# Kernel tuning notes

Hardware: AMD Instinct MI355X
Metric: run time of the kernel (lower is better)

Reference implementation:

```python
import jax, jax.numpy as jnp
import numpy as np
from jax import lax

B, N, S = 16, 8192, 512
BASE_K = 16
MS_K = (8, 16, 24)


def _fps(xyz, npoint):
    # farthest point sampling; xyz [B,N,3] -> indices [B,npoint]
    b, n, _ = xyz.shape
    def body(carry, _):
        dists, far = carry
        c = jnp.take_along_axis(xyz, far[:, None, None], axis=1)  # [B,1,3]
        d = jnp.sum((xyz - c) ** 2, -1)
        dists = jnp.minimum(dists, d)
        return (dists, jnp.argmax(dists, -1).astype(jnp.int32)), far
    init = (jnp.full((b, n), 1e10, xyz.dtype), jnp.zeros((b,), jnp.int32))
    _, idx = lax.scan(body, init, None, length=npoint)
    return idx.swapaxes(0, 1)  # [B,npoint]


def _sqdist(a, b):
    # a [B,S,3], b [B,N,3] -> squared distances [B,S,N] (same topk order as cdist)
    return (jnp.sum(a * a, -1)[:, :, None] + jnp.sum(b * b, -1)[:, None, :]
            - 2.0 * jnp.einsum('bsc,bnc->bsn', a, b))


def _gather(pts, idx):
    # pts [B,N,C], idx [B,S,K] -> [B,S,K,C]
    b = pts.shape[0]
    return pts[jnp.arange(b)[:, None, None], idx]


def setup_inputs():
    key = jax.random.key(0)
    ks = jax.random.split(key, 6)
    s = 0.05
    return {
        'l0_xyz': jax.random.normal(ks[0], (B, 3, N), jnp.float32),
        'l0_points': jax.random.normal(ks[1], (B, 3, N), jnp.float32),
        'sa_W1': jax.random.normal(ks[2], (64, 6), jnp.float32) * s,
        'sa_b1': jnp.zeros((64,), jnp.float32),
        'sa_W2': jax.random.normal(ks[3], (128, 64), jnp.float32) * s,
        'sa_b2': jnp.zeros((128,), jnp.float32),
        'ms_W1': jax.random.normal(ks[4], (3, 64, 3), jnp.float32) * s,
        'ms_b1': jnp.zeros((3, 64), jnp.float32),
        'ms_W2': jax.random.normal(ks[5], (3, 128, 64), jnp.float32) * s,
        'ms_b2': jnp.zeros((3, 128), jnp.float32),
    }


def reference(l0_xyz, l0_points, sa_W1, sa_b1, sa_W2, sa_b2, ms_W1, ms_b1, ms_W2, ms_b2):
    xyz = l0_xyz.swapaxes(1, 2)     # [B,N,3]
    pts = l0_points.swapaxes(1, 2)  # [B,N,3]
    # --- PointNet_SA_Module_KNN: FPS + KNN grouping + shared MLP + max-pool ---
    fps_idx = _fps(lax.stop_gradient(xyz), S)                         # [B,S]
    new_xyz = jnp.take_along_axis(xyz, fps_idx[:, :, None], axis=1)  # [B,S,3]
    d = _sqdist(lax.stop_gradient(new_xyz), lax.stop_gradient(xyz))  # [B,S,N]
    _, knn_idx = lax.top_k(-d, BASE_K)                                # [B,S,K]
    g_xyz = _gather(xyz, knn_idx) - new_xyz[:, :, None]               # [B,S,K,3]
    g_pts = _gather(pts, knn_idx)                                     # [B,S,K,3]
    feat = jnp.concatenate([g_xyz, g_pts], -1)                        # [B,S,K,6]
    h = jax.nn.relu(jnp.einsum('bskc,oc->bsko', feat, sa_W1) + sa_b1)
    h = jnp.einsum('bsko,po->bskp', h, sa_W2) + sa_b2
    base_feat = jnp.max(h, axis=2)                                    # [B,S,128]
    keypoints = new_xyz.swapaxes(1, 2)                                # [B,3,S]
    # --- multi-scale: no_grad cdist, per-scale topk + rel-coord MLP + max-pool ---
    dist = _sqdist(lax.stop_gradient(new_xyz), lax.stop_gradient(xyz))  # [B,S,N]
    feats = [base_feat.swapaxes(1, 2)]                                  # [B,128,S]
    for i, k in enumerate(MS_K):
        k_eff = min(k, N)
        _, idx = lax.top_k(-dist, k_eff)                                # [B,S,k]
        rel = _gather(xyz, idx) - new_xyz[:, :, None]                   # [B,S,k,3]
        h = jax.nn.relu(jnp.einsum('bskc,oc->bsko', rel, ms_W1[i]) + ms_b1[i])
        h = jnp.einsum('bsko,po->bskp', h, ms_W2[i]) + ms_b2[i]
        feats.append(jnp.max(h, axis=2).swapaxes(1, 2))                 # [B,128,S]
    return keypoints, jnp.concatenate(feats, axis=1)                    # [B,3,S],[B,512,S]
```

## Files before the change

### kernel.cpp

```cpp
#include <hip/hip_runtime.h>

#define BB 16
#define NN 8192
#define SS 512
#define N3 (3 * NN)
#define KD 14

typedef unsigned short u16;
typedef unsigned int u32;
typedef unsigned long long u64;
typedef float v2f __attribute__((ext_vector_type(2)));

__device__ __forceinline__ v2f pk_add(v2f a, v2f b) {
  v2f r;
  asm("v_pk_add_f32 %0, %1, %2" : "=v"(r) : "v"(a), "v"(b));
  return r;
}
__device__ __forceinline__ v2f pk_mul(v2f a, v2f b) {
  v2f r;
  asm("v_pk_mul_f32 %0, %1, %2" : "=v"(r) : "v"(a), "v"(b));
  return r;
}

template <int CTRL>
__device__ __forceinline__ u64 dpp_maxk(u64 k) {
  u32 lo = (u32)k, hi = (u32)(k >> 32);
  u32 slo = (u32)__builtin_amdgcn_update_dpp(0, (int)lo, CTRL, 0xf, 0xf, false);
  u32 shi = (u32)__builtin_amdgcn_update_dpp(0, (int)hi, CTRL, 0xf, 0xf, false);
  u64 s = ((u64)shi << 32) | (u64)slo;
  return (s > k) ? s : k;
}
__device__ __forceinline__ u64 maxk(u64 a, u64 b) { return (a > b) ? a : b; }

__global__ __launch_bounds__(256) void k_prep(const float* __restrict__ xyz,
                                              const float* __restrict__ pts,
                                              float4* __restrict__ xyz4,
                                              float4* __restrict__ pts4) {
  int i = blockIdx.x * 256 + threadIdx.x;
  int b = i >> 13, n = i & (NN - 1);
  const float* xb = xyz + b * N3;
  float x = xb[n], y = xb[NN + n], z = xb[2 * NN + n];
  float w = __fadd_rn(__fadd_rn(__fmul_rn(x, x), __fmul_rn(y, y)), __fmul_rn(z, z));
  xyz4[i] = make_float4(x, y, z, w);
  const float* pb = pts + b * N3;
  pts4[i] = make_float4(pb[n], pb[NN + n], pb[2 * NN + n], 0.f);
}

__global__ __attribute__((amdgpu_flat_work_group_size(512, 512),
                          amdgpu_waves_per_eu(2, 2)))
void k_fps(const float* __restrict__ xyz, float* __restrict__ out_kp) {
  __shared__ float sxyz[NN * 3];
  __shared__ int sIdx[SS];
  __shared__ u64 rkey[2][8];
  int b = blockIdx.x, t = threadIdx.x;
  const float* base = xyz + b * N3;
  v2f px[8], py[8], pz[8], dm[8];
#pragma unroll
  for (int j = 0; j < 8; ++j) {
    int n0 = j * 1024 + t, n1 = n0 + 512;
    px[j] = v2f{base[n0], base[n1]};
    py[j] = v2f{base[NN + n0], base[NN + n1]};
    pz[j] = v2f{base[2 * NN + n0], base[2 * NN + n1]};
    dm[j] = v2f{1e10f, 1e10f};
    sxyz[n0 * 3 + 0] = px[j].x;
    sxyz[n0 * 3 + 1] = py[j].x;
    sxyz[n0 * 3 + 2] = pz[j].x;
    sxyz[n1 * 3 + 0] = px[j].y;
    sxyz[n1 * 3 + 1] = py[j].y;
    sxyz[n1 * 3 + 2] = pz[j].y;
  }
#pragma unroll
  for (int j = 0; j < 8; ++j) {
    asm volatile("" : "+v"(px[j]), "+v"(py[j]), "+v"(pz[j]));
  }
  float cx = base[0], cy = base[NN], cz = base[2 * NN];
  int far = 0;
  int lane = t & 63, w = t >> 6;
  u32 tb = (u32)(NN - t);
  for (int it = 0; it < SS; ++it) {
    if (t == 0) sIdx[it] = far;
    v2f ncx = v2f{-cx, -cx}, ncy = v2f{-cy, -cy}, ncz = v2f{-cz, -cz};
    float vmax = 0.0f;
#pragma unroll
    for (int j = 0; j < 8; ++j) {
      v2f dx = pk_add(px[j], ncx);
      v2f dy = pk_add(py[j], ncy);
      v2f dz = pk_add(pz[j], ncz);
      v2f xx = pk_mul(dx, dx);
      v2f yy = pk_mul(dy, dy);
      v2f s = pk_add(xx, yy);
      v2f zz = pk_mul(dz, dz);
      v2f d = pk_add(s, zz);
      float a0 = fminf(dm[j].x, d.x);
      float a1 = fminf(dm[j].y, d.y);
      dm[j].x = a0;
      dm[j].y = a1;
      vmax = fmaxf(vmax, fmaxf(a0, a1));
    }
    u32 cand = 0;
#pragma unroll
    for (int j = 7; j >= 0; --j) {
      u32 v1 = tb - (u32)(j * 1024 + 512);
      u32 v0 = tb - (u32)(j * 1024);
      cand = (dm[j].y == vmax) ? v1 : cand;
      cand = (dm[j].x == vmax) ? v0 : cand;
    }
    u64 key = ((u64)__float_as_uint(vmax) << 32) | cand;
    key = dpp_maxk<0x111>(key);
    key = dpp_maxk<0x112>(key);
    key = dpp_maxk<0x114>(key);
    key = dpp_maxk<0x118>(key);
    key = dpp_maxk<0x142>(key);
    key = dpp_maxk<0x143>(key);
    int pb = it & 1;
    if (lane == 63) rkey[pb][w] = key;
    __syncthreads();
    u64 k0 = rkey[pb][0], k1 = rkey[pb][1];
    u64 k2 = rkey[pb][2], k3 = rkey[pb][3];
    u64 k4 = rkey[pb][4], k5 = rkey[pb][5];
    u64 k6 = rkey[pb][6], k7 = rkey[pb][7];
    u64 kg = maxk(maxk(maxk(k0, k1), maxk(k2, k3)),
                  maxk(maxk(k4, k5), maxk(k6, k7)));
    far = NN - (int)(u32)(kg & 0xffffffffu);
    cx = sxyz[far * 3 + 0];
    cy = sxyz[far * 3 + 1];
    cz = sxyz[far * 3 + 2];
  }
  __syncthreads();
  for (int i = t; i < SS; i += 512) {
    int id = sIdx[i];
    out_kp[b * 1536 + i] = base[id];
    out_kp[b * 1536 + SS + i] = base[NN + id];
    out_kp[b * 1536 + 2 * SS + i] = base[2 * NN + id];
  }
}

template <int USE4>
__global__ __launch_bounds__(256) void k_knn(const float* __restrict__ xyz,
                                             const float4* __restrict__ xyz4,
                                             const float* __restrict__ kp,
                                             u16* __restrict__ knn) {
  int t = threadIdx.x;
  int row = blockIdx.x * 4 + (t >> 6);
  int lane = t & 63;
  int b = row >> 9, s = row & (SS - 1);
  const float* base = xyz + b * N3;
  const float4* base4 = xyz4 + (b << 13);
  float ax = kp[b * 1536 + s];
  float ay = kp[b * 1536 + SS + s];
  float az = kp[b * 1536 + 2 * SS + s];
  float aw = __fadd_rn(__fadd_rn(__fmul_rn(ax, ax), __fmul_rn(ay, ay)), __fmul_rn(az, az));
  u64 arr[KD];
#pragma unroll
  for (int i = 0; i < KD; ++i) arr[i] = ~0ull;
  for (int c = 0; c < 128; ++c) {
    int n = c * 64 + lane;
    float qx, qy, qz, qw;
    if constexpr (USE4) {
      float4 q = base4[n];
      qx = q.x; qy = q.y; qz = q.z; qw = q.w;
    } else {
      qx = base[n]; qy = base[NN + n]; qz = base[2 * NN + n];
      qw = __fadd_rn(__fadd_rn(__fmul_rn(qx, qx), __fmul_rn(qy, qy)), __fmul_rn(qz, qz));
    }
    float dot = __fadd_rn(__fadd_rn(__fmul_rn(ax, qx), __fmul_rn(ay, qy)), __fmul_rn(az, qz));
    float d = __fsub_rn(__fadd_rn(aw, qw), __fmul_rn(2.0f, dot));
    u32 ub = __float_as_uint(d);
    ub ^= (ub & 0x80000000u) ? 0xFFFFFFFFu : 0x80000000u;
    u64 key = ((u64)ub << 32) | (u32)n;
    if (key < arr[KD - 1]) {
      bool cg[KD];
#pragma unroll
      for (int i = 0; i < KD; ++i) cg[i] = arr[i] > key;
#pragma unroll
      for (int i = KD - 1; i >= 1; --i)
        arr[i] = cg[i - 1] ? arr[i - 1] : (cg[i] ? key : arr[i]);
      arr[0] = cg[0] ? key : arr[0];
    }
  }
  u64 mine = 0;
  for (int it = 0; it < 24; ++it) {
    u64 m = arr[0];
#pragma unroll
    for (int off = 1; off < 64; off <<= 1) {
      u64 o = __shfl_xor(m, off, 64);
      m = (o < m) ? o : m;
    }
    if (lane == it) mine = m;
    if (arr[0] == m) {
#pragma unroll
      for (int i = 0; i < KD - 1; ++i) arr[i] = arr[i + 1];
      arr[KD - 1] = ~0ull;
    }
  }
  if (lane < 24) knn[row * 24 + lane] = (u16)(mine & 0xFFFFu);
}

template <int USE4>
__global__ __launch_bounds__(256) void k_mlp(
    const float* __restrict__ xyz, const float* __restrict__ pts,
    const float4* __restrict__ xyz4, const float4* __restrict__ pts4,
    const float* __restrict__ kp, const u16* __restrict__ knn,
    const float* __restrict__ W1, const float* __restrict__ b1,
    const float* __restrict__ W2, const float* __restrict__ b2,
    const float* __restrict__ msW1, const float* __restrict__ msb1,
    const float* __restrict__ msW2, const float* __restrict__ msb2,
    float* __restrict__ out) {
  __shared__ float smem[6688];
  int t = threadIdx.x, lane = t & 63, w = t >> 6;
  int b = blockIdx.x >> 6, s0 = (blockIdx.x & 63) * 8;
  if (blockIdx.y == 0) {
    float* sW1T = smem;
    float* sb1 = smem + 384;
    float* sfeat = smem + 448;
    float* sh1 = smem + 832;
    for (int i = t; i < 384; i += 256) {
      int o = i / 6, c = i - o * 6;
      sW1T[c * 64 + o] = W1[i];
    }
    if (t < 64) sb1[t] = b1[t];
    float wgtA[64], wgtB[64];
#pragma unroll
    for (int j = 0; j < 64; ++j) {
      wgtA[j] = W2[lane * 64 + j];
      wgtB[j] = W2[(lane + 64) * 64 + j];
    }
    float b2A = b2[lane], b2B = b2[lane + 64];
    __syncthreads();
    for (int g = 0; g < 2; ++g) {
      if (t < 128) {
        int p = t >> 1, h = t & 1;
        int rr = p >> 4, k = p & 15;
        int s = s0 + g * 4 + rr, row = b * SS + s;
        int id = knn[row * 24 + k];
        float* f = &sfeat[rr * 96 + k * 6];
        if (h == 0) {
          float qx, qy, qz;
          if constexpr (USE4) {
            float4 q = xyz4[(b << 13) + id];
            qx = q.x; qy = q.y; qz = q.z;
          } else {
            qx = xyz[b * N3 + id];
            qy = xyz[b * N3 + NN + id];
            qz = xyz[b * N3 + 2 * NN + id];
          }
          f[0] = __fsub_rn(qx, kp[b * 1536 + s]);
          f[1] = __fsub_rn(qy, kp[b * 1536 + SS + s]);
          f[2] = __fsub_rn(qz, kp[b * 1536 + 2 * SS + s]);
        } else {
          float px_, py_, pz_;
          if constexpr (USE4) {
            float4 q = pts4[(b << 13) + id];
            px_ = q.x; py_ = q.y; pz_ = q.z;
          } else {
            px_ = pts[b * N3 + id];
            py_ = pts[b * N3 + NN + id];
            pz_ = pts[b * N3 + 2 * NN + id];
          }
          f[3] = px_;
          f[4] = py_;
          f[5] = pz_;
        }
      }
      __syncthreads();
#pragma unroll
      for (int m = 0; m < 16; ++m) {
        int u = m * 256 + t;
        int rr = u >> 10, rem = u & 1023, k = rem >> 6, o = rem & 63;
        float acc = sb1[o];
#pragma unroll
        for (int c = 0; c < 6; ++c) acc = fmaf(sfeat[rr * 96 + k * 6 + c], sW1T[c * 64 + o], acc);
        sh1[rr * 1024 + k * 64 + o] = fmaxf(acc, 0.f);
      }
      __syncthreads();
      float bestA = -1e30f, bestB = -1e30f;
#pragma unroll
      for (int k = 0; k < 16; ++k) {
        const float4* h4 = (const float4*)&sh1[w * 1024 + k * 64];
        float a0 = 0.f, a1 = 0.f;
#pragma unroll
        for (int j = 0; j < 16; ++j) {
          float4 hv = h4[j];
          a0 = fmaf(hv.x, wgtA[4 * j], a0);
          a0 = fmaf(hv.y, wgtA[4 * j + 1], a0);
          a0 = fmaf(hv.z, wgtA[4 * j + 2], a0);
          a0 = fmaf(hv.w, wgtA[4 * j + 3], a0);
          a1 = fmaf(hv.x, wgtB[4 * j], a1);
          a1 = fmaf(hv.y, wgtB[4 * j + 1], a1);
          a1 = fmaf(hv.z, wgtB[4 * j + 2], a1);
          a1 = fmaf(hv.w, wgtB[4 * j + 3], a1);
        }
        bestA = fmaxf(bestA, a0);
        bestB = fmaxf(bestB, a1);
      }
      int s = s0 + g * 4 + w;
      out[24576 + b * 262144 + lane * 512 + s] = bestA + b2A;
      out[24576 + b * 262144 + (lane + 64) * 512 + s] = bestB + b2B;
      __syncthreads();
    }
  } else {
    int scale = blockIdx.y - 1;
    int kk = 8 * (scale + 1);
    float* sW1T = smem;
    float* sb1 = smem + 192;
    float* sfeat = smem + 256;
    float* sh1 = smem + 544;
    const float* W1s = msW1 + scale * 192;
    for (int i = t; i < 192; i += 256) {
      int o = i / 3, c = i - o * 3;
      sW1T[c * 64 + o] = W1s[i];
    }
    if (t < 64) sb1[t] = msb1[scale * 64 + t];
    float wgtA[64], wgtB[64];
#pragma unroll
    for (int j = 0; j < 64; ++j) {
      wgtA[j] = msW2[scale * 8192 + lane * 64 + j];
      wgtB[j] = msW2[scale * 8192 + (lane + 64) * 64 + j];
    }
    float b2A = msb2[scale * 128 + lane], b2B = msb2[scale * 128 + lane + 64];
    __syncthreads();
    int co = 128 * (scale + 1);
    for (int g = 0; g < 2; ++g) {
      if (t < 96) {
        int rr = t / 24, k = t - rr * 24;
        int s = s0 + g * 4 + rr, row = b * SS + s;
        int id = knn[row * 24 + k];
        float qx, qy, qz;
        if constexpr (USE4) {
          float4 q = xyz4[(b << 13) + id];
          qx = q.x; qy = q.y; qz = q.z;
        } else {
          qx = xyz[b * N3 + id];
          qy = xyz[b * N3 + NN + id];
          qz = xyz[b * N3 + 2 * NN + id];
        }
        float* f = &sfeat[rr * 72 + k * 3];
        f[0] = __fsub_rn(qx, kp[b * 1536 + s]);
        f[1] = __fsub_rn(qy, kp[b * 1536 + SS + s]);
        f[2] = __fsub_rn(qz, kp[b * 1536 + 2 * SS + s]);
      }
      __syncthreads();
      for (int rr = 0; rr < 4; ++rr) {
        for (int u = t; u < kk * 64; u += 256) {
          int k = u >> 6, o = u & 63;
          float acc = sb1[o];
          acc = fmaf(sfeat[rr * 72 + k * 3 + 0], sW1T[o], acc);
          acc = fmaf(sfeat[rr * 72 + k * 3 + 1], sW1T[64 + o], acc);
          acc = fmaf(sfeat[rr * 72 + k * 3 + 2], sW1T[128 + o], acc);
          sh1[rr * 1536 + k * 64 + o] = fmaxf(acc, 0.f);
        }
      }
      __syncthreads();
      float bestA = -1e30f, bestB = -1e30f;
      for (int k = 0; k < kk; ++k) {
        const float4* h4 = (const float4*)&sh1[w * 1536 + k * 64];
        float a0 = 0.f, a1 = 0.f;
#pragma unroll
        for (int j = 0; j < 16; ++j) {
          float4 hv = h4[j];
          a0 = fmaf(hv.x, wgtA[4 * j], a0);
          a0 = fmaf(hv.y, wgtA[4 * j + 1], a0);
          a0 = fmaf(hv.z, wgtA[4 * j + 2], a0);
          a0 = fmaf(hv.w, wgtA[4 * j + 3], a0);
          a1 = fmaf(hv.x, wgtB[4 * j], a1);
          a1 = fmaf(hv.y, wgtB[4 * j + 1], a1);
          a1 = fmaf(hv.z, wgtB[4 * j + 2], a1);
          a1 = fmaf(hv.w, wgtB[4 * j + 3], a1);
        }
        bestA = fmaxf(bestA, a0);
        bestB = fmaxf(bestB, a1);
      }
      int s = s0 + g * 4 + w;
      out[24576 + b * 262144 + (co + lane) * 512 + s] = bestA + b2A;
      out[24576 + b * 262144 + (co + lane + 64) * 512 + s] = bestB + b2B;
      __syncthreads();
    }
  }
}

extern "C" void kernel_launch(void* const* d_in, const int* in_sizes, int n_in,
                              void* d_out, int out_size, void* d_ws, size_t ws_size,
                              hipStream_t stream) {
  const float* xyz = (const float*)d_in[0];
  const float* pts = (const float*)d_in[1];
  const float* sa_W1 = (const float*)d_in[2];
  const float* sa_b1 = (const float*)d_in[3];
  const float* sa_W2 = (const float*)d_in[4];
  const float* sa_b2 = (const float*)d_in[5];
  const float* ms_W1 = (const float*)d_in[6];
  const float* ms_b1 = (const float*)d_in[7];
  const float* ms_W2 = (const float*)d_in[8];
  const float* ms_b2 = (const float*)d_in[9];
  float* out = (float*)d_out;
  const float* kp = (const float*)d_out;

  u16* knn = (u16*)d_ws;
  float4* xyz4 = (float4*)((char*)d_ws + 393216);
  float4* pts4 = xyz4 + BB * NN;
  const size_t need4 = 393216 + (size_t)2 * BB * NN * sizeof(float4);
  const bool use4 = ws_size >= need4;

  if (use4) k_prep<<<BB * NN / 256, 256, 0, stream>>>(xyz, pts, xyz4, pts4);
  k_fps<<<BB, 512, 0, stream>>>(xyz, out);
  if (use4) {
    k_knn<1><<<(BB * SS) / 4, 256, 0, stream>>>(xyz, xyz4, kp, knn);
    k_mlp<1><<<dim3(BB * 64, 4), 256, 0, stream>>>(xyz, pts, xyz4, pts4, kp, knn,
                                                   sa_W1, sa_b1, sa_W2, sa_b2,
                                                   ms_W1, ms_b1, ms_W2, ms_b2, out);
  } else {
    k_knn<0><<<(BB * SS) / 4, 256, 0, stream>>>(xyz, xyz4, kp, knn);
    k_mlp<0><<<dim3(BB * 64, 4), 256, 0, stream>>>(xyz, pts, xyz4, pts4, kp, knn,
                                                   sa_W1, sa_b1, sa_W2, sa_b2,
                                                   ms_W1, ms_b1, ms_W2, ms_b2, out);
  }
}
```

Measured before the change: 967.1 us.

## Fuse FPS and KNN into one persistent kernel with progress flags

FPS and KNN now run in a single launch. The 16 FPS blocks publish each sampled keypoint and bump a per-batch progress counter. The extra 128 worker blocks spin on those counters and compute top-k neighbours for each keypoint as soon as it exists. This overlaps the serial FPS loop with the KNN work, instead of running KNN only after all of FPS finishes. It relies on all blocks being co-resident (there is a deadlock risk if they are not), and it adds global stores, memory fences and spin-wait traffic inside the FPS loop.

```diff
diff --git a/kernel.cpp b/kernel.cpp
--- a/kernel.cpp
+++ b/kernel.cpp
@@ -5,6 +5,8 @@
 #define SS 512
 #define N3 (3 * NN)
 #define KD 14
+#define KNN_BLOCKS 128
+#define KNN_WAVES (KNN_BLOCKS * 8)
 
 typedef unsigned short u16;
 typedef unsigned int u32;
@@ -35,7 +37,11 @@
 __global__ __launch_bounds__(256) void k_prep(const float* __restrict__ xyz,
                                               const float* __restrict__ pts,
                                               float4* __restrict__ xyz4,
-                                              float4* __restrict__ pts4) {
+                                              float4* __restrict__ pts4,
+                                              u32* __restrict__ progress) {
+  if (blockIdx.x == 0 && threadIdx.x < BB)
+    __hip_atomic_store(progress + threadIdx.x, 0u, __ATOMIC_RELAXED,
+                       __HIP_MEMORY_SCOPE_AGENT);
   int i = blockIdx.x * 256 + threadIdx.x;
   int b = i >> 13, n = i & (NN - 1);
   const float* xb = xyz + b * N3;
@@ -48,7 +54,169 @@
 
 __global__ __attribute__((amdgpu_flat_work_group_size(512, 512),
                           amdgpu_waves_per_eu(2, 2)))
-void k_fps(const float* __restrict__ xyz, float* __restrict__ out_kp) {
+void k_fps_knn(const float* __restrict__ xyz, const float4* __restrict__ xyz4,
+               float* __restrict__ out_kp, u16* __restrict__ knn,
+               u32* __restrict__ progress) {
+  __shared__ float sxyz[NN * 3];
+  __shared__ u64 rkey[2][8];
+  int t = threadIdx.x;
+  int lane = t & 63, w = t >> 6;
+  if (blockIdx.x < BB) {
+    int b = blockIdx.x;
+    const float* base = xyz + b * N3;
+    v2f px[8], py[8], pz[8], dm[8];
+#pragma unroll
+    for (int j = 0; j < 8; ++j) {
+      int n0 = j * 1024 + t, n1 = n0 + 512;
+      px[j] = v2f{base[n0], base[n1]};
+      py[j] = v2f{base[NN + n0], base[NN + n1]};
+      pz[j] = v2f{base[2 * NN + n0], base[2 * NN + n1]};
+      dm[j] = v2f{1e10f, 1e10f};
+      sxyz[n0 * 3 + 0] = px[j].x;
+      sxyz[n0 * 3 + 1] = py[j].x;
+      sxyz[n0 * 3 + 2] = pz[j].x;
+      sxyz[n1 * 3 + 0] = px[j].y;
+      sxyz[n1 * 3 + 1] = py[j].y;
+      sxyz[n1 * 3 + 2] = pz[j].y;
+    }
+#pragma unroll
+    for (int j = 0; j < 8; ++j) {
+      asm volatile("" : "+v"(px[j]), "+v"(py[j]), "+v"(pz[j]));
+    }
+    float cx = base[0], cy = base[NN], cz = base[2 * NN];
+    u32 tb = (u32)(NN - t);
+    for (int it = 0; it < SS; ++it) {
+      if (t == 0) {
+        if (it > 0) {
+          asm volatile("s_waitcnt vmcnt(0)" ::: "memory");
+          __hip_atomic_store(progress + b, (u32)it, __ATOMIC_RELAXED,
+                             __HIP_MEMORY_SCOPE_AGENT);
+        }
+        __hip_atomic_store(out_kp + b * 1536 + it, cx, __ATOMIC_RELAXED,
+                           __HIP_MEMORY_SCOPE_AGENT);
+        __hip_atomic_store(out_kp + b * 1536 + SS + it, cy, __ATOMIC_RELAXED,
+                           __HIP_MEMORY_SCOPE_AGENT);
+        __hip_atomic_store(out_kp + b * 1536 + 2 * SS + it, cz, __ATOMIC_RELAXED,
+                           __HIP_MEMORY_SCOPE_AGENT);
+      }
+      v2f ncx = v2f{-cx, -cx}, ncy = v2f{-cy, -cy}, ncz = v2f{-cz, -cz};
+      float vmax = 0.0f;
+#pragma unroll
+      for (int j = 0; j < 8; ++j) {
+        v2f dx = pk_add(px[j], ncx);
+        v2f dy = pk_add(py[j], ncy);
+        v2f dz = pk_add(pz[j], ncz);
+        v2f xx = pk_mul(dx, dx);
+        v2f yy = pk_mul(dy, dy);
+        v2f s = pk_add(xx, yy);
+        v2f zz = pk_mul(dz, dz);
+        v2f d = pk_add(s, zz);
+        float a0 = fminf(dm[j].x, d.x);
+        float a1 = fminf(dm[j].y, d.y);
+        dm[j].x = a0;
+        dm[j].y = a1;
+        vmax = fmaxf(vmax, fmaxf(a0, a1));
+      }
+      u32 cand = 0;
+#pragma unroll
+      for (int j = 7; j >= 0; --j) {
+        u32 v1 = tb - (u32)(j * 1024 + 512);
+        u32 v0 = tb - (u32)(j * 1024);
+        cand = (dm[j].y == vmax) ? v1 : cand;
+        cand = (dm[j].x == vmax) ? v0 : cand;
+      }
+      u64 key = ((u64)__float_as_uint(vmax) << 32) | cand;
+      key = dpp_maxk<0x111>(key);
+      key = dpp_maxk<0x112>(key);
+      key = dpp_maxk<0x114>(key);
+      key = dpp_maxk<0x118>(key);
+      key = dpp_maxk<0x142>(key);
+      key = dpp_maxk<0x143>(key);
+      int pb = it & 1;
+      if (lane == 63) rkey[pb][w] = key;
+      __syncthreads();
+      u64 k0 = rkey[pb][0], k1 = rkey[pb][1];
+      u64 k2 = rkey[pb][2], k3 = rkey[pb][3];
+      u64 k4 = rkey[pb][4], k5 = rkey[pb][5];
+      u64 k6 = rkey[pb][6], k7 = rkey[pb][7];
+      u64 kg = maxk(maxk(maxk(k0, k1), maxk(k2, k3)),
+                    maxk(maxk(k4, k5), maxk(k6, k7)));
+      int far = NN - (int)(u32)(kg & 0xffffffffu);
+      cx = sxyz[far * 3 + 0];
+      cy = sxyz[far * 3 + 1];
+      cz = sxyz[far * 3 + 2];
+    }
+    if (t == 0) {
+      asm volatile("s_waitcnt vmcnt(0)" ::: "memory");
+      __hip_atomic_store(progress + b, (u32)SS, __ATOMIC_RELAXED,
+                         __HIP_MEMORY_SCOPE_AGENT);
+    }
+  } else {
+    int wg = (blockIdx.x - BB) * 8 + w;
+    for (int pass = 0; pass < 8; ++pass) {
+      int wid = wg + pass * KNN_WAVES;
+      int s = wid >> 4, b = wid & 15;
+      if (lane == 0) {
+        while (__hip_atomic_load(progress + b, __ATOMIC_ACQUIRE,
+                                 __HIP_MEMORY_SCOPE_AGENT) <= (u32)s)
+          __builtin_amdgcn_s_sleep(2);
+      }
+      asm volatile("" ::: "memory");
+      float ax = __hip_atomic_load(out_kp + b * 1536 + s, __ATOMIC_RELAXED,
+                                   __HIP_MEMORY_SCOPE_AGENT);
+      float ay = __hip_atomic_load(out_kp + b * 1536 + SS + s, __ATOMIC_RELAXED,
+                                   __HIP_MEMORY_SCOPE_AGENT);
+      float az = __hip_atomic_load(out_kp + b * 1536 + 2 * SS + s, __ATOMIC_RELAXED,
+                                   __HIP_MEMORY_SCOPE_AGENT);
+      float aw = __fadd_rn(__fadd_rn(__fmul_rn(ax, ax), __fmul_rn(ay, ay)),
+                           __fmul_rn(az, az));
+      const float4* base4 = xyz4 + (b << 13);
+      u64 arr[KD];
+#pragma unroll
+      for (int i = 0; i < KD; ++i) arr[i] = ~0ull;
+      for (int c = 0; c < 128; ++c) {
+        int n = c * 64 + lane;
+        float4 q = base4[n];
+        float dot = __fadd_rn(__fadd_rn(__fmul_rn(ax, q.x), __fmul_rn(ay, q.y)),
+                              __fmul_rn(az, q.z));
+        float d = __fsub_rn(__fadd_rn(aw, q.w), __fmul_rn(2.0f, dot));
+        u32 ub = __float_as_uint(d);
+        ub ^= (ub & 0x80000000u) ? 0xFFFFFFFFu : 0x80000000u;
+        u64 key = ((u64)ub << 32) | (u32)n;
+        if (key < arr[KD - 1]) {
+          bool cg[KD];
+#pragma unroll
+          for (int i = 0; i < KD; ++i) cg[i] = arr[i] > key;
+#pragma unroll
+          for (int i = KD - 1; i >= 1; --i)
+            arr[i] = cg[i - 1] ? arr[i - 1] : (cg[i] ? key : arr[i]);
+          arr[0] = cg[0] ? key : arr[0];
+        }
+      }
+      u64 mine = 0;
+      for (int it = 0; it < 24; ++it) {
+        u64 m = arr[0];
+#pragma unroll
+        for (int off = 1; off < 64; off <<= 1) {
+          u64 o = __shfl_xor(m, off, 64);
+          m = (o < m) ? o : m;
+        }
+        if (lane == it) mine = m;
+        if (arr[0] == m) {
+#pragma unroll
+          for (int i = 0; i < KD - 1; ++i) arr[i] = arr[i + 1];
+          arr[KD - 1] = ~0ull;
+        }
+      }
+      int row = b * SS + s;
+      if (lane < 24) knn[row * 24 + lane] = (u16)(mine & 0xFFFFu);
+    }
+  }
+}
+
+__global__ __attribute__((amdgpu_flat_work_group_size(512, 512),
+                          amdgpu_waves_per_eu(2, 2)))
+void k_fps_solo(const float* __restrict__ xyz, float* __restrict__ out_kp) {
   __shared__ float sxyz[NN * 3];
   __shared__ int sIdx[SS];
   __shared__ u64 rkey[2][8];
@@ -70,9 +238,7 @@
     sxyz[n1 * 3 + 2] = pz[j].y;
   }
 #pragma unroll
-  for (int j = 0; j < 8; ++j) {
-    asm volatile("" : "+v"(px[j]), "+v"(py[j]), "+v"(pz[j]));
-  }
+  for (int j = 0; j < 8; ++j) asm volatile("" : "+v"(px[j]), "+v"(py[j]), "+v"(pz[j]));
   float cx = base[0], cy = base[NN], cz = base[2 * NN];
   int far = 0;
   int lane = t & 63, w = t >> 6;
@@ -135,17 +301,14 @@
   }
 }
 
-template <int USE4>
-__global__ __launch_bounds__(256) void k_knn(const float* __restrict__ xyz,
-                                             const float4* __restrict__ xyz4,
-                                             const float* __restrict__ kp,
-                                             u16* __restrict__ knn) {
+__global__ __launch_bounds__(256) void k_knn_solo(const float* __restrict__ xyz,
+                                                  const float* __restrict__ kp,
+                                                  u16* __restrict__ knn) {
   int t = threadIdx.x;
   int row = blockIdx.x * 4 + (t >> 6);
   int lane = t & 63;
   int b = row >> 9, s = row & (SS - 1);
   const float* base = xyz + b * N3;
-  const float4* base4 = xyz4 + (b << 13);
   float ax = kp[b * 1536 + s];
   float ay = kp[b * 1536 + SS + s];
   float az = kp[b * 1536 + 2 * SS + s];
@@ -155,14 +318,8 @@
   for (int i = 0; i < KD; ++i) arr[i] = ~0ull;
   for (int c = 0; c < 128; ++c) {
     int n = c * 64 + lane;
-    float qx, qy, qz, qw;
-    if constexpr (USE4) {
-      float4 q = base4[n];
-      qx = q.x; qy = q.y; qz = q.z; qw = q.w;
-    } else {
-      qx = base[n]; qy = base[NN + n]; qz = base[2 * NN + n];
-      qw = __fadd_rn(__fadd_rn(__fmul_rn(qx, qx), __fmul_rn(qy, qy)), __fmul_rn(qz, qz));
-    }
+    float qx = base[n], qy = base[NN + n], qz = base[2 * NN + n];
+    float qw = __fadd_rn(__fadd_rn(__fmul_rn(qx, qx), __fmul_rn(qy, qy)), __fmul_rn(qz, qz));
     float dot = __fadd_rn(__fadd_rn(__fmul_rn(ax, qx), __fmul_rn(ay, qy)), __fmul_rn(az, qz));
     float d = __fsub_rn(__fadd_rn(aw, qw), __fmul_rn(2.0f, dot));
     u32 ub = __float_as_uint(d);
@@ -397,18 +554,19 @@
   u16* knn = (u16*)d_ws;
   float4* xyz4 = (float4*)((char*)d_ws + 393216);
   float4* pts4 = xyz4 + BB * NN;
-  const size_t need4 = 393216 + (size_t)2 * BB * NN * sizeof(float4);
-  const bool use4 = ws_size >= need4;
-
-  if (use4) k_prep<<<BB * NN / 256, 256, 0, stream>>>(xyz, pts, xyz4, pts4);
-  k_fps<<<BB, 512, 0, stream>>>(xyz, out);
-  if (use4) {
-    k_knn<1><<<(BB * SS) / 4, 256, 0, stream>>>(xyz, xyz4, kp, knn);
+  u32* progress = (u32*)(pts4 + BB * NN);
+  const size_t need = 393216 + (size_t)2 * BB * NN * sizeof(float4) + 64;
+  const bool fused = ws_size >= need;
+
+  if (fused) {
+    k_prep<<<BB * NN / 256, 256, 0, stream>>>(xyz, pts, xyz4, pts4, progress);
+    k_fps_knn<<<BB + KNN_BLOCKS, 512, 0, stream>>>(xyz, xyz4, out, knn, progress);
     k_mlp<1><<<dim3(BB * 64, 4), 256, 0, stream>>>(xyz, pts, xyz4, pts4, kp, knn,
                                                    sa_W1, sa_b1, sa_W2, sa_b2,
                                                    ms_W1, ms_b1, ms_W2, ms_b2, out);
   } else {
-    k_knn<0><<<(BB * SS) / 4, 256, 0, stream>>>(xyz, xyz4, kp, knn);
+    k_fps_solo<<<BB, 512, 0, stream>>>(xyz, out);
+    k_knn_solo<<<(BB * SS) / 4, 256, 0, stream>>>(xyz, kp, knn);
     k_mlp<0><<<dim3(BB * 64, 4), 256, 0, stream>>>(xyz, pts, xyz4, pts4, kp, knn,
                                                    sa_W1, sa_b1, sa_W2, sa_b2,
                                                    ms_W1, ms_b1, ms_W2, ms_b2, out);
```

New measurement: 1.051 ms. +8.7%, slower.
